# Optimization experiments

Hardware: AMD Instinct MI355X
Metric: run time of the kernel (lower is better)

Reference implementation:

```python
import jax, jax.numpy as jnp
from jax import lax
import numpy as np
import math

B, H, W, C = 4, 32, 256, 96
EXPAND, N, R, K = 2, 16, 6, 2
DI = EXPAND * C


def setup_inputs() -> dict:
    key = jax.random.key(0)
    ks = jax.random.split(key, 10)
    x = jax.random.normal(ks[0], (B, H, W, C), jnp.float32)
    W_in = jax.random.normal(ks[1], (2 * DI, C), jnp.float32) * (C ** -0.5)
    conv_w = jax.random.normal(ks[2], (DI, 1, 3, 3), jnp.float32) * (1.0 / 3.0)
    conv_b = jnp.zeros((DI,), jnp.float32)
    x_proj_weight = jax.random.normal(ks[3], (K, R + 2 * N, DI), jnp.float32) * (DI ** -0.5)
    dt_init_std = R ** -0.5
    dt_projs_weight = jax.random.uniform(ks[4], (K, DI, R), jnp.float32, -dt_init_std, dt_init_std)
    dt_min, dt_max = 1e-3, 1e-1
    dt = jnp.exp(jax.random.uniform(ks[5], (K, DI), jnp.float32) * (math.log(dt_max) - math.log(dt_min)) + math.log(dt_min))
    dt = jnp.clip(dt, 1e-4, None)
    dt_projs_bias = dt + jnp.log(-jnp.expm1(-dt))
    A_logs = jnp.tile(jnp.log(jnp.arange(1, N + 1, dtype=jnp.float32))[None, :], (K * DI, 1))
    Ds = jnp.ones((K * DI,), jnp.float32)
    W_out = jax.random.normal(ks[6], (C, DI), jnp.float32) * (DI ** -0.5)
    return {"x": x, "W_in": W_in, "conv_w": conv_w, "conv_b": conv_b,
            "x_proj_weight": x_proj_weight, "dt_projs_weight": dt_projs_weight,
            "dt_projs_bias": dt_projs_bias, "A_logs": A_logs, "Ds": Ds, "W_out": W_out}


def reference(x, W_in, conv_w, conv_b, x_proj_weight, dt_projs_weight,
              dt_projs_bias, A_logs, Ds, W_out):
    Bb, Hh, Ww, Cc = x.shape
    DIi = conv_w.shape[0]
    Kk = x_proj_weight.shape[0]
    Nn = A_logs.shape[-1]
    Rr = dt_projs_weight.shape[-1]
    L = Hh * Ww

    # in_proj + chunk
    xz = x @ W_in.T                       # (B,H,W,2*DI)
    xc, z = xz[..., :DIi], xz[..., DIi:]
    # depthwise conv (NCHW)
    xc = jnp.transpose(xc, (0, 3, 1, 2))
    xc = lax.conv_general_dilated(xc, conv_w, (1, 1), 'SAME',
                                  dimension_numbers=('NCHW', 'OIHW', 'NCHW'),
                                  feature_group_count=DIi)
    xc = jax.nn.silu(xc + conv_b[None, :, None, None])

    # cross-scan: forward + reversed (K=2)
    xf = xc.reshape(Bb, DIi, L)
    xs = jnp.stack([xf, xf[..., ::-1]], axis=1)          # (B,K,DI,L)

    x_dbl = jnp.einsum('bkdl,kcd->bkcl', xs, x_proj_weight)
    dts_r = x_dbl[:, :, :Rr]                             # (B,K,R,L)
    Bs = x_dbl[:, :, Rr:Rr + Nn]                         # (B,K,N,L)
    Cs = x_dbl[:, :, Rr + Nn:]                           # (B,K,N,L)
    dts = jnp.einsum('bkrl,kdr->bkdl', dts_r, dt_projs_weight)

    As = -jnp.exp(A_logs).reshape(Kk, DIi, Nn)           # (K,DI,N)
    Dd = Ds.reshape(Kk, DIi)
    delta = jax.nn.softplus(dts + dt_projs_bias.reshape(1, Kk, DIi, 1))

    # sequential selective scan over L
    u_t = jnp.moveaxis(xs, -1, 0)      # (L,B,K,DI)
    d_t = jnp.moveaxis(delta, -1, 0)   # (L,B,K,DI)
    B_t = jnp.moveaxis(Bs, -1, 0)      # (L,B,K,N)
    C_t = jnp.moveaxis(Cs, -1, 0)      # (L,B,K,N)

    def step(h, inp):
        u, dlt, Bt, Ct = inp
        dA = jnp.exp(dlt[..., None] * As)                       # (B,K,DI,N)
        h = dA * h + (dlt * u)[..., None] * Bt[:, :, None, :]
        y = jnp.sum(h * Ct[:, :, None, :], axis=-1)             # (B,K,DI)
        return h, y

    h0 = jnp.zeros((Bb, Kk, DIi, Nn), x.dtype)
    _, ys = lax.scan(step, h0, (u_t, d_t, B_t, C_t))
    ys = jnp.moveaxis(ys, 0, -1)                                # (B,K,DI,L)
    ys = ys + xs * Dd[None, :, :, None]

    # un-flip reversed direction and merge
    y = ys[:, 0] + ys[:, 1][..., ::-1]                          # (B,DI,L)
    y = jnp.transpose(y.reshape(Bb, DIi, Hh, Ww), (0, 2, 3, 1)) # (B,H,W,DI)

    out = (y * jax.nn.silu(z)) @ W_out.T                        # (B,H,W,C)
    return out
```

## Files before the change

### kernel.cpp

```cpp
#include <hip/hip_runtime.h>

constexpr int Bb = 4, Hh = 32, Wd = 256, Cc = 96;
constexpr int DI = 192, Nn = 16, Rr = 6, Kk = 2;
constexpr int LL = Hh * Wd;
constexpr int ROWS = Bb * LL;
constexpr int PROJ_C = 40;
constexpr int G = 128;
constexpr int CH = LL / G;
constexpr int SEG = 16;
constexpr int SL = G / SEG;
constexpr size_t YSZ = (size_t)Bb * DI * LL;

static __device__ __forceinline__ float sigmoidf_(float v) {
  return 1.f / (1.f + __expf(-v));
}

__global__ __launch_bounds__(256) void k_xz(const float* __restrict__ x,
                                            const float* __restrict__ Win,
                                            float* __restrict__ xc,
                                            float* __restrict__ zbuf) {
  __shared__ float As[32][132];
  __shared__ float Ws[32][100];
  const int tid = threadIdx.x;
  const int row0 = blockIdx.x * 128;
  const int c0 = blockIdx.y * 96;
  const int tx = tid & 7;
  const int ty = tid >> 3;
  float acc[4][12] = {};

  for (int kc = 0; kc < 3; ++kc) {
    const int d0 = kc * 32;
    __syncthreads();
    for (int v = tid; v < 1024; v += 256) {
      const int l = v >> 3, dk4 = v & 7;
      const float4 xv =
          *(const float4*)&x[(size_t)(row0 + l) * 96 + d0 + dk4 * 4];
      As[dk4 * 4 + 0][l] = xv.x;
      As[dk4 * 4 + 1][l] = xv.y;
      As[dk4 * 4 + 2][l] = xv.z;
      As[dk4 * 4 + 3][l] = xv.w;
    }
    for (int v = tid; v < 768; v += 256) {
      const int c = v >> 3, dk4 = v & 7;
      const float4 wv =
          *(const float4*)&Win[(size_t)(c0 + c) * 96 + d0 + dk4 * 4];
      Ws[dk4 * 4 + 0][c] = wv.x;
      Ws[dk4 * 4 + 1][c] = wv.y;
      Ws[dk4 * 4 + 2][c] = wv.z;
      Ws[dk4 * 4 + 3][c] = wv.w;
    }
    __syncthreads();
    for (int dk = 0; dk < 32; ++dk) {
      const float4 a4 = *(const float4*)&As[dk][ty * 4];
      const float4 w0 = *(const float4*)&Ws[dk][tx * 12];
      const float4 w1 = *(const float4*)&Ws[dk][tx * 12 + 4];
      const float4 w2 = *(const float4*)&Ws[dk][tx * 12 + 8];
      const float av[4] = {a4.x, a4.y, a4.z, a4.w};
      const float wv[12] = {w0.x, w0.y, w0.z, w0.w, w1.x, w1.y,
                            w1.z, w1.w, w2.x, w2.y, w2.z, w2.w};
#pragma unroll
      for (int i = 0; i < 4; ++i)
#pragma unroll
        for (int j = 0; j < 12; ++j)
          acc[i][j] = fmaf(av[i], wv[j], acc[i][j]);
    }
  }

  float* dst;
  int cc0;
  if (c0 < DI) { dst = xc; cc0 = c0; }
  else         { dst = zbuf; cc0 = c0 - DI; }
#pragma unroll
  for (int i = 0; i < 4; ++i) {
    float* op = dst + (size_t)(row0 + ty * 4 + i) * DI + cc0 + tx * 12;
    *(float4*)(op + 0) = make_float4(acc[i][0], acc[i][1], acc[i][2], acc[i][3]);
    *(float4*)(op + 4) = make_float4(acc[i][4], acc[i][5], acc[i][6], acc[i][7]);
    *(float4*)(op + 8) = make_float4(acc[i][8], acc[i][9], acc[i][10], acc[i][11]);
  }
}

__global__ __launch_bounds__(256) void k_conv(const float* __restrict__ xc,
                                              const float* __restrict__ cw,
                                              const float* __restrict__ cbias,
                                              float* __restrict__ xf) {
  __shared__ float wl[9 * DI];
  __shared__ float bl[DI];
  const int tid = threadIdx.x;
  for (int v = tid; v < 9 * DI; v += 256) {
    int dd = v / 9, t = v % 9;
    wl[t * DI + dd] = cw[v];
  }
  if (tid < DI) bl[tid] = cbias[tid];
  __syncthreads();

  int gid = blockIdx.x * 256 + tid;
  int d4 = gid % 48;
  int rem = gid / 48;
  int w4 = rem % 64;
  int bh = rem / 64;
  int h = bh % Hh, b = bh / Hh;
  const int d0 = d4 * 4, w0 = w4 * 4;

  float4 c[3][6];
#pragma unroll
  for (int dr = 0; dr < 3; ++dr) {
    const int h2 = h + dr - 1;
    const bool hv = (unsigned)h2 < (unsigned)Hh;
    const int hc = hv ? h2 : h;
    const float* rp = xc + ((size_t)(b * LL + (hc << 8))) * DI + d0;
#pragma unroll
    for (int j = 0; j < 6; ++j) {
      const int wc = w0 - 1 + j;
      const bool wv = (unsigned)wc < (unsigned)Wd;
      const int wcc = wv ? wc : w0;
      float4 v = *(const float4*)&rp[(size_t)wcc * DI];
      const float m = (hv && wv) ? 1.f : 0.f;
      c[dr][j] = make_float4(v.x * m, v.y * m, v.z * m, v.w * m);
    }
  }

  float4 wv9[9];
#pragma unroll
  for (int t = 0; t < 9; ++t) wv9[t] = *(const float4*)&wl[t * DI + d0];
  const float4 bias4 = *(const float4*)&bl[d0];

#pragma unroll
  for (int wi = 0; wi < 4; ++wi) {
    float4 a = bias4;
#pragma unroll
    for (int dr = 0; dr < 3; ++dr)
#pragma unroll
      for (int dc = 0; dc < 3; ++dc) {
        const float4 vv = c[dr][wi + dc];
        const float4 ww = wv9[dr * 3 + dc];
        a.x = fmaf(vv.x, ww.x, a.x);
        a.y = fmaf(vv.y, ww.y, a.y);
        a.z = fmaf(vv.z, ww.z, a.z);
        a.w = fmaf(vv.w, ww.w, a.w);
      }
    float4 r;
    r.x = a.x * sigmoidf_(a.x);
    r.y = a.y * sigmoidf_(a.y);
    r.z = a.z * sigmoidf_(a.z);
    r.w = a.w * sigmoidf_(a.w);
    *(float4*)&xf[((size_t)(b * LL + (h << 8) + w0 + wi)) * DI + d0] = r;
  }
}

__global__ __launch_bounds__(256) void k_proj(const float* __restrict__ xf,
                                              const float* __restrict__ xpw,
                                              float* __restrict__ proj) {
  __shared__ float smem[5376];
  float* As = smem;
  float* Ws = smem + 32 * 68;
  const int tid = threadIdx.x;
  const int row0 = blockIdx.x * 64;
  const int b = row0 >> 13;
  const int l0 = row0 & (LL - 1);
  const int tx = tid & 15;
  const int ty = tid >> 4;
  float acc[4][5] = {};

  for (int kc = 0; kc < 6; ++kc) {
    const int d0 = kc * 32;
    __syncthreads();
    for (int v = tid; v < 512; v += 256) {
      const int l = v >> 3, dk4 = v & 7;
      const float4 xv =
          *(const float4*)&xf[((size_t)b * LL + l0 + l) * DI + d0 + dk4 * 4];
      As[(dk4 * 4 + 0) * 68 + l] = xv.x;
      As[(dk4 * 4 + 1) * 68 + l] = xv.y;
      As[(dk4 * 4 + 2) * 68 + l] = xv.z;
      As[(dk4 * 4 + 3) * 68 + l] = xv.w;
    }
    for (int v = tid; v < 640; v += 256) {
      const int s = v >> 3, dk4 = v & 7;
      const int k = s / 40, off = s % 40;
      float4 wv = make_float4(0.f, 0.f, 0.f, 0.f);
      if (off < 6 || off >= 8) {
        const int c = off < 6 ? off : off - 2;
        wv = *(const float4*)&xpw[(size_t)(k * 38 + c) * DI + d0 + dk4 * 4];
      }
      Ws[(dk4 * 4 + 0) * 84 + s] = wv.x;
      Ws[(dk4 * 4 + 1) * 84 + s] = wv.y;
      Ws[(dk4 * 4 + 2) * 84 + s] = wv.z;
      Ws[(dk4 * 4 + 3) * 84 + s] = wv.w;
    }
    __syncthreads();
    for (int dk = 0; dk < 32; ++dk) {
      const float4 a4 = *(const float4*)&As[dk * 68 + ty * 4];
      float w[5];
#pragma unroll
      for (int j = 0; j < 5; ++j) w[j] = Ws[dk * 84 + tx * 5 + j];
      const float av[4] = {a4.x, a4.y, a4.z, a4.w};
#pragma unroll
      for (int i = 0; i < 4; ++i)
#pragma unroll
        for (int j = 0; j < 5; ++j)
          acc[i][j] = fmaf(av[i], w[j], acc[i][j]);
    }
  }

  __syncthreads();
  float* res = smem;
#pragma unroll
  for (int i = 0; i < 4; ++i)
#pragma unroll
    for (int j = 0; j < 5; ++j)
      res[(ty * 4 + i) * 84 + tx * 5 + j] = acc[i][j];
  __syncthreads();
#pragma unroll
  for (int k = 0; k < 2; ++k) {
    float* dst = proj + ((size_t)(b * Kk + k) * LL + l0) * PROJ_C;
    for (int v = tid; v < 640; v += 256) {
      const int l = v / 10, q = v % 10;
      *(float4*)&dst[l * PROJ_C + q * 4] =
          *(const float4*)&res[l * 84 + k * 40 + q * 4];
    }
  }
}

template <int PASS, int KDIR>
static __device__ __forceinline__ void scan_block(
    const float* __restrict__ proj, const float* __restrict__ xf,
    const float* __restrict__ dtw, const float* __restrict__ dtb,
    const float* __restrict__ Dsv, const float* __restrict__ hinit,
    float* __restrict__ smry, float* __restrict__ yout, const int b,
    const int g) {
  constexpr int PSTP = KDIR ? -PROJ_C : PROJ_C;
  constexpr int DIS = KDIR ? -DI : DI;
  const int d = threadIdx.x;
  const int kd = KDIR * DI + d;
  const int bk = b * Kk + KDIR;

  float w6[6];
#pragma unroll
  for (int r = 0; r < 6; ++r) w6[r] = dtw[kd * 6 + r];
  const float dbias = dtb[kd];
  const float Dv = (PASS == 3) ? Dsv[kd] : 0.f;

  const size_t hbase = (((size_t)(bk * G + g)) * DI + d) * Nn;
  float h[16];
  if (PASS == 1) {
#pragma unroll
    for (int n = 0; n < 16; ++n) h[n] = 0.f;
  } else {
#pragma unroll
    for (int j = 0; j < 4; ++j) {
      const float4 h4 = *(const float4*)&hinit[hbase + 4 * j];
      h[4 * j + 0] = h4.x;
      h[4 * j + 1] = h4.y;
      h[4 * j + 2] = h4.z;
      h[4 * j + 3] = h4.w;
    }
  }

  const int l0 = KDIR ? (LL - 1 - g * CH) : (g * CH);
  const float* Pr = proj + ((size_t)bk * LL + l0) * PROJ_C;
  const float* up = xf + ((size_t)b * LL + l0) * DI + d;
  float* yw = nullptr;
  if (PASS == 3)
    yw = yout + (size_t)KDIR * YSZ + ((size_t)b * LL + l0) * DI + d;

  float dsum = 0.f;
  float u8[8];
#pragma unroll
  for (int i = 0; i < 8; ++i) u8[i] = up[i * DIS];

  for (int t0 = 0; t0 < CH; t0 += 8) {
    const bool pre = (t0 + 8) < CH;
#pragma unroll
    for (int j = 0; j < 8; ++j) {
      const int t = t0 + j;
      const float u = u8[j];
      if (pre) u8[j] = up[(t + 8) * DIS];
      const float* P = Pr + t * PSTP;
      const float4 p0 = *(const float4*)P;
      const float2 p1 = *(const float2*)(P + 4);
      float vr = dbias;
      vr = fmaf(p0.x, w6[0], vr);
      vr = fmaf(p0.y, w6[1], vr);
      vr = fmaf(p0.z, w6[2], vr);
      vr = fmaf(p0.w, w6[3], vr);
      vr = fmaf(p1.x, w6[4], vr);
      vr = fmaf(p1.y, w6[5], vr);
      const float ex = __expf(vr);
      const float dlt = (vr > 20.f) ? vr : __logf(1.f + ex);
      const float E = __builtin_amdgcn_rcpf(1.f + ex);
      if (PASS == 1) dsum += dlt;
      const float du = dlt * u;
      const float E2 = E * E, E4 = E2 * E2, E8 = E4 * E4;
      const float fbs[4] = {E, E4 * E, E8 * E, E8 * E4 * E};
      float yp = 0.f, yq = 0.f;
#pragma unroll
      for (int jj = 0; jj < 4; ++jj) {
        float f = fbs[jj];
        const float4 Bj = *(const float4*)(P + 8 + 4 * jj);
        h[4 * jj + 0] = fmaf(f, h[4 * jj + 0], du * Bj.x);
        f *= E;
        h[4 * jj + 1] = fmaf(f, h[4 * jj + 1], du * Bj.y);
        f *= E;
        h[4 * jj + 2] = fmaf(f, h[4 * jj + 2], du * Bj.z);
        f *= E;
        h[4 * jj + 3] = fmaf(f, h[4 * jj + 3], du * Bj.w);
        if (PASS == 3) {
          const float4 Cj = *(const float4*)(P + 24 + 4 * jj);
          yp = fmaf(h[4 * jj + 0], Cj.x, yp);
          yq = fmaf(h[4 * jj + 1], Cj.y, yq);
          yp = fmaf(h[4 * jj + 2], Cj.z, yp);
          yq = fmaf(h[4 * jj + 3], Cj.w, yq);
        }
      }
      if (PASS == 3) yw[t * DIS] = fmaf(u, Dv, yp + yq);
    }
  }

  if (PASS == 1) {
    const float Es = __expf(-dsum);
    float Pn = Es;
    const size_t sb = hbase * 2;
#pragma unroll
    for (int j = 0; j < 4; ++j) {
      float4 v0, v1;
      v0.x = Pn; v0.y = h[4 * j + 0]; Pn *= Es;
      v0.z = Pn; v0.w = h[4 * j + 1]; Pn *= Es;
      v1.x = Pn; v1.y = h[4 * j + 2]; Pn *= Es;
      v1.z = Pn; v1.w = h[4 * j + 3]; Pn *= Es;
      *(float4*)&smry[sb + 8 * j] = v0;
      *(float4*)&smry[sb + 8 * j + 4] = v1;
    }
  }
}

template <int PASS>
__global__ __launch_bounds__(192) void k_scan(
    const float* __restrict__ proj, const float* __restrict__ xf,
    const float* __restrict__ dtw, const float* __restrict__ dtb,
    const float* __restrict__ Dsv, const float* __restrict__ hinit,
    float* __restrict__ smry, float* __restrict__ yout) {
  int bid = blockIdx.x;
  const int kdir = bid & 1;
  bid >>= 1;
  const int g = bid & (G - 1);
  bid >>= 7;
  const int b = bid;

  if (kdir == 0)
    scan_block<PASS, 0>(proj, xf, dtw, dtb, Dsv, hinit, smry, yout, b, g);
  else
    scan_block<PASS, 1>(proj, xf, dtw, dtb, Dsv, hinit, smry, yout, b, g);
}

__global__ __launch_bounds__(256) void k_s2a(const float* __restrict__ smry,
                                             float* __restrict__ segPH) {
  const int idx = blockIdx.x * 256 + threadIdx.x;
  const int n = idx & 15;
  int rem = idx >> 4;
  const int d = rem % DI;
  rem /= DI;
  const int seg = rem % SEG;
  const int bk = rem / SEG;
  float P = 1.f, H = 0.f;
#pragma unroll 4
  for (int q = 0; q < SL; ++q) {
    const int g = seg * SL + q;
    const size_t hb = (((size_t)(bk * G + g)) * DI + d) * Nn + n;
    const float2 ph = *(const float2*)&smry[hb * 2];
    H = fmaf(ph.x, H, ph.y);
    P *= ph.x;
  }
  const size_t sa = (((size_t)(bk * SEG + seg) * DI + d) * Nn + n) * 2;
  *(float2*)&segPH[sa] = make_float2(P, H);
}

__global__ __launch_bounds__(256) void k_s2b(float* __restrict__ segPH) {
  const int idx = blockIdx.x * 256 + threadIdx.x;
  const int n = idx & 15;
  const int d = (idx >> 4) % DI;
  const int bk = idx / (16 * DI);
  float carry = 0.f;
#pragma unroll
  for (int s = 0; s < SEG; ++s) {
    const size_t a = (((size_t)(bk * SEG + s) * DI + d) * Nn + n) * 2;
    const float2 ph = *(const float2*)&segPH[a];
    segPH[a + 1] = carry;
    carry = fmaf(ph.x, carry, ph.y);
  }
}

__global__ __launch_bounds__(256) void k_s2c(const float* __restrict__ smry,
                                             const float* __restrict__ segPH,
                                             float* __restrict__ hini) {
  const int idx = blockIdx.x * 256 + threadIdx.x;
  const int n = idx & 15;
  int rem = idx >> 4;
  const int d = rem % DI;
  rem /= DI;
  const int seg = rem % SEG;
  const int bk = rem / SEG;
  float carry =
      segPH[(((size_t)(bk * SEG + seg) * DI + d) * Nn + n) * 2 + 1];
#pragma unroll 4
  for (int q = 0; q < SL; ++q) {
    const int g = seg * SL + q;
    const size_t hb = (((size_t)(bk * G + g)) * DI + d) * Nn + n;
    hini[hb] = carry;
    const float2 ph = *(const float2*)&smry[hb * 2];
    carry = fmaf(ph.x, carry, ph.y);
  }
}

__global__ __launch_bounds__(256) void k_out(const float* __restrict__ y,
                                             const float* __restrict__ zbuf,
                                             const float* __restrict__ Wout,
                                             float* __restrict__ out) {
  __shared__ float As[32][132];
  __shared__ float Ws[32][100];
  const int tid = threadIdx.x;
  const int row0 = blockIdx.x * 128;
  const int b = row0 >> 13;
  const int l0 = row0 & (LL - 1);
  const int tx = tid & 7;
  const int ty = tid >> 3;
  float acc[4][12] = {};

  for (int kc = 0; kc < 6; ++kc) {
    const int d0 = kc * 32;
    __syncthreads();
    for (int v = tid; v < 1024; v += 256) {
      const int l = v >> 3, dk4 = v & 7;
      const size_t idx = ((size_t)b * LL + l0 + l) * DI + d0 + dk4 * 4;
      const float4 zv = *(const float4*)&zbuf[idx];
      const float4 y0v = *(const float4*)&y[idx];
      const float4 y1v = *(const float4*)&y[YSZ + idx];
      As[dk4 * 4 + 0][l] = zv.x * sigmoidf_(zv.x) * (y0v.x + y1v.x);
      As[dk4 * 4 + 1][l] = zv.y * sigmoidf_(zv.y) * (y0v.y + y1v.y);
      As[dk4 * 4 + 2][l] = zv.z * sigmoidf_(zv.z) * (y0v.z + y1v.z);
      As[dk4 * 4 + 3][l] = zv.w * sigmoidf_(zv.w) * (y0v.w + y1v.w);
    }
    for (int v = tid; v < 768; v += 256) {
      const int c = v >> 3, dk4 = v & 7;
      const float4 wv = *(const float4*)&Wout[(size_t)c * DI + d0 + dk4 * 4];
      Ws[dk4 * 4 + 0][c] = wv.x;
      Ws[dk4 * 4 + 1][c] = wv.y;
      Ws[dk4 * 4 + 2][c] = wv.z;
      Ws[dk4 * 4 + 3][c] = wv.w;
    }
    __syncthreads();
    for (int dk = 0; dk < 32; ++dk) {
      const float4 a4 = *(const float4*)&As[dk][ty * 4];
      const float4 w0 = *(const float4*)&Ws[dk][tx * 12];
      const float4 w1 = *(const float4*)&Ws[dk][tx * 12 + 4];
      const float4 w2 = *(const float4*)&Ws[dk][tx * 12 + 8];
      const float av[4] = {a4.x, a4.y, a4.z, a4.w};
      const float wv[12] = {w0.x, w0.y, w0.z, w0.w, w1.x, w1.y,
                            w1.z, w1.w, w2.x, w2.y, w2.z, w2.w};
#pragma unroll
      for (int i = 0; i < 4; ++i)
#pragma unroll
        for (int j = 0; j < 12; ++j)
          acc[i][j] = fmaf(av[i], wv[j], acc[i][j]);
    }
  }

#pragma unroll
  for (int i = 0; i < 4; ++i) {
    float* op = out + ((size_t)b * LL + l0 + ty * 4 + i) * 96 + tx * 12;
    *(float4*)(op + 0) = make_float4(acc[i][0], acc[i][1], acc[i][2], acc[i][3]);
    *(float4*)(op + 4) = make_float4(acc[i][4], acc[i][5], acc[i][6], acc[i][7]);
    *(float4*)(op + 8) = make_float4(acc[i][8], acc[i][9], acc[i][10], acc[i][11]);
  }
}

extern "C" void kernel_launch(void* const* d_in, const int* in_sizes, int n_in,
                              void* d_out, int out_size, void* d_ws,
                              size_t ws_size, hipStream_t stream) {
  const float* x    = (const float*)d_in[0];
  const float* Win  = (const float*)d_in[1];
  const float* cw   = (const float*)d_in[2];
  const float* cb   = (const float*)d_in[3];
  const float* xpw  = (const float*)d_in[4];
  const float* dtw  = (const float*)d_in[5];
  const float* dtb  = (const float*)d_in[6];
  const float* Dsv  = (const float*)d_in[8];
  const float* Wout = (const float*)d_in[9];
  float* out = (float*)d_out;

  float* ws = (float*)d_ws;
  size_t o = 0;
  float* zbuf  = ws + o;  o += (size_t)ROWS * DI;
  float* xf    = ws + o;  o += (size_t)ROWS * DI;
  float* proj  = ws + o;  o += (size_t)Bb * Kk * LL * PROJ_C;
  const size_t hsz = (size_t)Bb * Kk * G * DI * Nn;
  float* smry  = ws + o;  o += 2 * hsz;
  float* hini  = ws + o;  o += hsz;
  float* segPH = ws + o;  o += (size_t)Bb * Kk * SEG * DI * Nn * 2;
  float* y     = ws + o;  o += 2 * YSZ;
  float* xc    = y;

  k_xz<<<dim3(ROWS / 128, 4), 256, 0, stream>>>(x, Win, xc, zbuf);
  k_conv<<<dim3((Bb * Hh * 64 * 48) / 256), 256, 0, stream>>>(xc, cw, cb, xf);
  k_proj<<<dim3(ROWS / 64), 256, 0, stream>>>(xf, xpw, proj);
  k_scan<1><<<dim3(Bb * Kk * G), 192, 0, stream>>>(
      proj, xf, dtw, dtb, Dsv, nullptr, smry, nullptr);
  k_s2a<<<dim3(Bb * Kk * SEG * DI * Nn / 256), 256, 0, stream>>>(smry, segPH);
  k_s2b<<<dim3(Bb * Kk * DI * Nn / 256), 256, 0, stream>>>(segPH);
  k_s2c<<<dim3(Bb * Kk * SEG * DI * Nn / 256), 256, 0, stream>>>(smry, segPH,
                                                                 hini);
  k_scan<3><<<dim3(Bb * Kk * G), 192, 0, stream>>>(
      proj, xf, dtw, dtb, Dsv, hini, nullptr, y);
  k_out<<<dim3(ROWS / 128), 256, 0, stream>>>(y, zbuf, Wout, out);
}
```

Measured before the change: 299.9 us.

## Compute chunk-local outputs in first scan pass, add carry correction pass

```diff
diff --git a/kernel.cpp b/kernel.cpp
--- a/kernel.cpp
+++ b/kernel.cpp
@@ -220,11 +220,11 @@
   }
 }
 
-template <int PASS, int KDIR>
-static __device__ __forceinline__ void scan_block(
+template <int KDIR>
+static __device__ __forceinline__ void scanF_block(
     const float* __restrict__ proj, const float* __restrict__ xf,
     const float* __restrict__ dtw, const float* __restrict__ dtb,
-    const float* __restrict__ Dsv, const float* __restrict__ hinit,
+    const float* __restrict__ Dsv, float* __restrict__ Dbuf,
     float* __restrict__ smry, float* __restrict__ yout, const int b,
     const int g) {
   constexpr int PSTP = KDIR ? -PROJ_C : PROJ_C;
@@ -237,30 +237,18 @@
 #pragma unroll
   for (int r = 0; r < 6; ++r) w6[r] = dtw[kd * 6 + r];
   const float dbias = dtb[kd];
-  const float Dv = (PASS == 3) ? Dsv[kd] : 0.f;
+  const float Dv = Dsv[kd];
 
   const size_t hbase = (((size_t)(bk * G + g)) * DI + d) * Nn;
   float h[16];
-  if (PASS == 1) {
-#pragma unroll
-    for (int n = 0; n < 16; ++n) h[n] = 0.f;
-  } else {
-#pragma unroll
-    for (int j = 0; j < 4; ++j) {
-      const float4 h4 = *(const float4*)&hinit[hbase + 4 * j];
-      h[4 * j + 0] = h4.x;
-      h[4 * j + 1] = h4.y;
-      h[4 * j + 2] = h4.z;
-      h[4 * j + 3] = h4.w;
-    }
-  }
+#pragma unroll
+  for (int n = 0; n < 16; ++n) h[n] = 0.f;
 
   const int l0 = KDIR ? (LL - 1 - g * CH) : (g * CH);
   const float* Pr = proj + ((size_t)bk * LL + l0) * PROJ_C;
   const float* up = xf + ((size_t)b * LL + l0) * DI + d;
-  float* yw = nullptr;
-  if (PASS == 3)
-    yw = yout + (size_t)KDIR * YSZ + ((size_t)b * LL + l0) * DI + d;
+  float* yw = yout + (size_t)KDIR * YSZ + ((size_t)b * LL + l0) * DI + d;
+  float* Dw = Dbuf + ((size_t)bk * LL + l0) * DI + d;
 
   float dsum = 0.f;
   float u8[8];
@@ -287,7 +275,8 @@
       const float ex = __expf(vr);
       const float dlt = (vr > 20.f) ? vr : __logf(1.f + ex);
       const float E = __builtin_amdgcn_rcpf(1.f + ex);
-      if (PASS == 1) dsum += dlt;
+      dsum += dlt;
+      Dw[t * DIS] = dsum;
       const float du = dlt * u;
       const float E2 = E * E, E4 = E2 * E2, E8 = E4 * E4;
       const float fbs[4] = {E, E4 * E, E8 * E, E8 * E4 * E};
@@ -303,40 +292,35 @@
         h[4 * jj + 2] = fmaf(f, h[4 * jj + 2], du * Bj.z);
         f *= E;
         h[4 * jj + 3] = fmaf(f, h[4 * jj + 3], du * Bj.w);
-        if (PASS == 3) {
-          const float4 Cj = *(const float4*)(P + 24 + 4 * jj);
-          yp = fmaf(h[4 * jj + 0], Cj.x, yp);
-          yq = fmaf(h[4 * jj + 1], Cj.y, yq);
-          yp = fmaf(h[4 * jj + 2], Cj.z, yp);
-          yq = fmaf(h[4 * jj + 3], Cj.w, yq);
-        }
+        const float4 Cj = *(const float4*)(P + 24 + 4 * jj);
+        yp = fmaf(h[4 * jj + 0], Cj.x, yp);
+        yq = fmaf(h[4 * jj + 1], Cj.y, yq);
+        yp = fmaf(h[4 * jj + 2], Cj.z, yp);
+        yq = fmaf(h[4 * jj + 3], Cj.w, yq);
       }
-      if (PASS == 3) yw[t * DIS] = fmaf(u, Dv, yp + yq);
-    }
-  }
-
-  if (PASS == 1) {
-    const float Es = __expf(-dsum);
-    float Pn = Es;
-    const size_t sb = hbase * 2;
-#pragma unroll
-    for (int j = 0; j < 4; ++j) {
-      float4 v0, v1;
-      v0.x = Pn; v0.y = h[4 * j + 0]; Pn *= Es;
-      v0.z = Pn; v0.w = h[4 * j + 1]; Pn *= Es;
-      v1.x = Pn; v1.y = h[4 * j + 2]; Pn *= Es;
-      v1.z = Pn; v1.w = h[4 * j + 3]; Pn *= Es;
-      *(float4*)&smry[sb + 8 * j] = v0;
-      *(float4*)&smry[sb + 8 * j + 4] = v1;
-    }
-  }
-}
-
-template <int PASS>
-__global__ __launch_bounds__(192) void k_scan(
+      yw[t * DIS] = fmaf(u, Dv, yp + yq);
+    }
+  }
+
+  const float Es = __expf(-dsum);
+  float Pn = Es;
+  const size_t sb = hbase * 2;
+#pragma unroll
+  for (int j = 0; j < 4; ++j) {
+    float4 v0, v1;
+    v0.x = Pn; v0.y = h[4 * j + 0]; Pn *= Es;
+    v0.z = Pn; v0.w = h[4 * j + 1]; Pn *= Es;
+    v1.x = Pn; v1.y = h[4 * j + 2]; Pn *= Es;
+    v1.z = Pn; v1.w = h[4 * j + 3]; Pn *= Es;
+    *(float4*)&smry[sb + 8 * j] = v0;
+    *(float4*)&smry[sb + 8 * j + 4] = v1;
+  }
+}
+
+__global__ __launch_bounds__(192) void k_scanF(
     const float* __restrict__ proj, const float* __restrict__ xf,
     const float* __restrict__ dtw, const float* __restrict__ dtb,
-    const float* __restrict__ Dsv, const float* __restrict__ hinit,
+    const float* __restrict__ Dsv, float* __restrict__ Dbuf,
     float* __restrict__ smry, float* __restrict__ yout) {
   int bid = blockIdx.x;
   const int kdir = bid & 1;
@@ -346,9 +330,9 @@
   const int b = bid;
 
   if (kdir == 0)
-    scan_block<PASS, 0>(proj, xf, dtw, dtb, Dsv, hinit, smry, yout, b, g);
+    scanF_block<0>(proj, xf, dtw, dtb, Dsv, Dbuf, smry, yout, b, g);
   else
-    scan_block<PASS, 1>(proj, xf, dtw, dtb, Dsv, hinit, smry, yout, b, g);
+    scanF_block<1>(proj, xf, dtw, dtb, Dsv, Dbuf, smry, yout, b, g);
 }
 
 __global__ __launch_bounds__(256) void k_s2a(const float* __restrict__ smry,
@@ -410,6 +394,78 @@
   }
 }
 
+template <int KDIR>
+static __device__ __forceinline__ void corr_block(
+    const float* __restrict__ proj, const float* __restrict__ Dbuf,
+    const float* __restrict__ hini, float* __restrict__ yout, const int b,
+    const int g) {
+  const int d = threadIdx.x;
+  const int bk = b * Kk + KDIR;
+  const int lm = KDIR ? (LL - (g + 1) * CH) : (g * CH);
+  const float* Pr = proj + ((size_t)bk * LL + lm) * PROJ_C;
+  const float* Dp = Dbuf + ((size_t)bk * LL + lm) * DI + d;
+  float* yb = yout + (size_t)KDIR * YSZ + ((size_t)b * LL + lm) * DI + d;
+
+  const size_t hb = (((size_t)(bk * G + g)) * DI + d) * Nn;
+  float hv[16];
+#pragma unroll
+  for (int j = 0; j < 4; ++j) {
+    const float4 h4 = *(const float4*)&hini[hb + 4 * j];
+    hv[4 * j + 0] = h4.x;
+    hv[4 * j + 1] = h4.y;
+    hv[4 * j + 2] = h4.z;
+    hv[4 * j + 3] = h4.w;
+  }
+
+  float D8[8];
+#pragma unroll
+  for (int i = 0; i < 8; ++i) D8[i] = Dp[i * DI];
+
+  for (int t0 = 0; t0 < CH; t0 += 8) {
+    const bool pre = (t0 + 8) < CH;
+#pragma unroll
+    for (int j = 0; j < 8; ++j) {
+      const int t = t0 + j;
+      const float D = D8[j];
+      if (pre) D8[j] = Dp[(t + 8) * DI];
+      const float Es = __expf(-D);
+      const float E2 = Es * Es, E4 = E2 * E2, E8 = E4 * E4;
+      const float fbs[4] = {Es, E4 * Es, E8 * Es, E8 * E4 * Es};
+      const float* P = Pr + t * PROJ_C;
+      float cp = 0.f, cq = 0.f;
+#pragma unroll
+      for (int jj = 0; jj < 4; ++jj) {
+        float f = fbs[jj];
+        const float4 Cj = *(const float4*)(P + 24 + 4 * jj);
+        cp = fmaf(f * hv[4 * jj + 0], Cj.x, cp);
+        f *= Es;
+        cq = fmaf(f * hv[4 * jj + 1], Cj.y, cq);
+        f *= Es;
+        cp = fmaf(f * hv[4 * jj + 2], Cj.z, cp);
+        f *= Es;
+        cq = fmaf(f * hv[4 * jj + 3], Cj.w, cq);
+      }
+      yb[t * DI] += cp + cq;
+    }
+  }
+}
+
+__global__ __launch_bounds__(192) void k_corr(
+    const float* __restrict__ proj, const float* __restrict__ Dbuf,
+    const float* __restrict__ hini, float* __restrict__ yout) {
+  int bid = blockIdx.x;
+  const int kdir = bid & 1;
+  bid >>= 1;
+  const int g = bid & (G - 1);
+  bid >>= 7;
+  const int b = bid;
+
+  if (kdir == 0)
+    corr_block<0>(proj, Dbuf, hini, yout, b, g);
+  else
+    corr_block<1>(proj, Dbuf, hini, yout, b, g);
+}
+
 __global__ __launch_bounds__(256) void k_out(const float* __restrict__ y,
                                              const float* __restrict__ zbuf,
                                              const float* __restrict__ Wout,
@@ -493,21 +549,21 @@
   float* proj  = ws + o;  o += (size_t)Bb * Kk * LL * PROJ_C;
   const size_t hsz = (size_t)Bb * Kk * G * DI * Nn;
   float* smry  = ws + o;  o += 2 * hsz;
-  float* hini  = ws + o;  o += hsz;
-  float* segPH = ws + o;  o += (size_t)Bb * Kk * SEG * DI * Nn * 2;
+  float* Dbuf  = ws + o;  o += (size_t)Bb * Kk * LL * DI;
   float* y     = ws + o;  o += 2 * YSZ;
   float* xc    = y;
+  float* hini  = xf;
+  float* segPH = xf + hsz;
 
   k_xz<<<dim3(ROWS / 128, 4), 256, 0, stream>>>(x, Win, xc, zbuf);
   k_conv<<<dim3((Bb * Hh * 64 * 48) / 256), 256, 0, stream>>>(xc, cw, cb, xf);
   k_proj<<<dim3(ROWS / 64), 256, 0, stream>>>(xf, xpw, proj);
-  k_scan<1><<<dim3(Bb * Kk * G), 192, 0, stream>>>(
-      proj, xf, dtw, dtb, Dsv, nullptr, smry, nullptr);
+  k_scanF<<<dim3(Bb * Kk * G), 192, 0, stream>>>(proj, xf, dtw, dtb, Dsv,
+                                                 Dbuf, smry, y);
   k_s2a<<<dim3(Bb * Kk * SEG * DI * Nn / 256), 256, 0, stream>>>(smry, segPH);
   k_s2b<<<dim3(Bb * Kk * DI * Nn / 256), 256, 0, stream>>>(segPH);
   k_s2c<<<dim3(Bb * Kk * SEG * DI * Nn / 256), 256, 0, stream>>>(smry, segPH,
                                                                  hini);
-  k_scan<3><<<dim3(Bb * Kk * G), 192, 0, stream>>>(
-      proj, xf, dtw, dtb, Dsv, hini, nullptr, y);
+  k_corr<<<dim3(Bb * Kk * G), 192, 0, stream>>>(proj, Dbuf, hini, y);
   k_out<<<dim3(ROWS / 128), 256, 0, stream>>>(y, zbuf, Wout, out);
 }
```

New measurement: 313.6 us. 1.05x slower.
